# Kernel optimization log

Measured on AMD Instinct MI355X. Metric: run time of the kernel, lower is better.

Reference implementation:

```python
import jax, jax.numpy as jnp
import numpy as np

D_MODEL = 1024
N_HEADS = 16
D_K = D_MODEL // N_HEADS


def setup_inputs() -> dict:
    key = jax.random.key(0)
    ks = jax.random.split(key, 9)
    B, S = 4, 2048
    scale = 0.02
    x = jax.random.normal(ks[0], (B, S, D_MODEL), dtype=jnp.float32)
    mask = jnp.ones((1, 1, S, S), dtype=jnp.int32)
    wq = jax.random.normal(ks[1], (D_MODEL, D_MODEL), dtype=jnp.float32) * scale
    bq = jnp.zeros((D_MODEL,), dtype=jnp.float32)
    wk = jax.random.normal(ks[2], (D_MODEL, D_MODEL), dtype=jnp.float32) * scale
    bk = jnp.zeros((D_MODEL,), dtype=jnp.float32)
    wv = jax.random.normal(ks[3], (D_MODEL, D_MODEL), dtype=jnp.float32) * scale
    bv = jnp.zeros((D_MODEL,), dtype=jnp.float32)
    wo = jax.random.normal(ks[4], (D_MODEL, D_MODEL), dtype=jnp.float32) * scale
    bo = jnp.zeros((D_MODEL,), dtype=jnp.float32)
    return {"x": x, "mask": mask, "wq": wq, "bq": bq, "wk": wk, "bk": bk,
            "wv": wv, "bv": bv, "wo": wo, "bo": bo}


def reference(x, mask, wq, bq, wk, bk, wv, bv, wo, bo):
    B, S, _ = x.shape
    # torch Linear: y = x @ W.T + b
    def proj(w, b):
        return (jnp.einsum('bsd,ed->bse', x, w) + b).reshape(B, S, N_HEADS, D_K).transpose(0, 2, 1, 3)
    q = proj(wq, bq)  # [B,H,S,Dk]
    k = proj(wk, bk)
    v = proj(wv, bv)
    scores = jnp.einsum('bhqd,bhkd->bhqk', q, k) / jnp.sqrt(jnp.float32(D_K))
    scores = jnp.where(mask == 0, jnp.float32(-jnp.inf), scores)
    attn = jax.nn.softmax(scores, axis=-1)
    out = jnp.einsum('bhqk,bhkd->bhqd', attn, v)  # [B,H,S,Dk]
    out = out.transpose(0, 2, 1, 3).reshape(B, S, D_MODEL)
    return jnp.einsum('bsd,ed->bse', out, wo) + bo
```

## Files before the change

kernel.cpp:

```cpp
#include <hip/hip_runtime.h>
#include <hip/hip_bf16.h>
#include <math.h>
#include <stdint.h>

typedef unsigned short u16;
typedef unsigned int u32;
typedef __bf16 bf16x2 __attribute__((ext_vector_type(2)));
typedef __bf16 bf16x8 __attribute__((ext_vector_type(8)));
typedef float f32x4 __attribute__((ext_vector_type(4)));

#define AS1 __attribute__((address_space(1)))
#define AS3 __attribute__((address_space(3)))

#define QSCALE 0.18033688011112042f

__device__ __forceinline__ u16 f2bf(float f) {
  union { float f; u32 i; } c; c.f = f;
  const u32 x = c.i;
  return (u16)((x + 0x7fffu + ((x >> 16) & 1u)) >> 16);
}
#if __has_builtin(__builtin_amdgcn_cvt_pk_bf16_f32)
__device__ __forceinline__ u32 pkbf(float a, float b) {
  const bf16x2 v = __builtin_amdgcn_cvt_pk_bf16_f32(a, b);
  union { bf16x2 v; u32 i; } c; c.v = v; return c.i;
}
#else
__device__ __forceinline__ u32 pkbf(float a, float b) {
  return (u32)f2bf(a) | ((u32)f2bf(b) << 16);
}
#endif
#if __has_builtin(__builtin_amdgcn_exp2f)
#define EXP2(x) __builtin_amdgcn_exp2f(x)
#else
#define EXP2(x) __expf((x) * 0.6931471805599453f)
#endif
__device__ __forceinline__ void gload_lds16(const void* g, void* lds) {
  __builtin_amdgcn_global_load_lds((const AS1 void*)g, (AS3 void*)lds, 16, 0, 0);
}

__global__ void cast_all_kernel(const float* __restrict__ x, const float* __restrict__ wq,
                                const float* __restrict__ wk, const float* __restrict__ wv,
                                const float* __restrict__ wo, u16* __restrict__ xh,
                                u16* __restrict__ wh) {
  const int i = blockIdx.x * 256 + threadIdx.x;
  const float* src; u16* dst; int off;
  if (i < 2097152) {
    src = x; dst = xh; off = i;
  } else {
    const int j = i - 2097152;
    const int w = j >> 18;
    off = j & 262143;
    src = (w == 0) ? wq : (w == 1) ? wk : (w == 2) ? wv : wo;
    dst = wh + (size_t)w * 1048576;
  }
  const float4 v = ((const float4*)src)[off];
  ushort4 o;
  o.x = f2bf(v.x); o.y = f2bf(v.y); o.z = f2bf(v.z); o.w = f2bf(v.w);
  ((ushort4*)dst)[off] = o;
}

template <int MODE, bool SCALE>
__device__ __forceinline__ void gemm_body(const u16* __restrict__ A,
                                          const u16* __restrict__ W,
                                          const float* __restrict__ bias,
                                          void* __restrict__ out) {
  __shared__ alignas(16) u16 As[128 * 32];
  __shared__ alignas(16) u16 Bs[128 * 32];
  const int tid = threadIdx.x;
  const int wave = tid >> 6, lane = tid & 63;
  const int quad = lane >> 4, l16 = lane & 15;
  const int m0 = blockIdx.y * 128, n0 = blockIdx.x * 128;
  const int wm = (wave >> 1) * 64, wn = (wave & 1) * 64;

  f32x4 vzero = {0.f, 0.f, 0.f, 0.f};
  f32x4 acc[4][4];
#pragma unroll
  for (int i = 0; i < 4; i++)
#pragma unroll
    for (int j = 0; j < 4; j++) acc[i][j] = vzero;

  for (int k0 = 0; k0 < 1024; k0 += 32) {
#pragma unroll
    for (int p = 0; p < 2; ++p) {
      const int cbase = p * 256 + wave * 64;
      const int c = cbase + lane;
      const int row = c >> 2, kc4 = c & 3;
      gload_lds16(A + (size_t)(m0 + row) * 1024 + k0 + kc4 * 8, (char*)As + cbase * 16);
      gload_lds16(W + (size_t)(n0 + row) * 1024 + k0 + kc4 * 8, (char*)Bs + cbase * 16);
    }
    __syncthreads();
    bf16x8 af[4], bw[4];
#pragma unroll
    for (int im = 0; im < 4; im++)
      af[im] = *(const bf16x8*)&As[(wm + im * 16 + l16) * 32 + quad * 8];
#pragma unroll
    for (int in_ = 0; in_ < 4; in_++)
      bw[in_] = *(const bf16x8*)&Bs[(wn + in_ * 16 + l16) * 32 + quad * 8];
#pragma unroll
    for (int im = 0; im < 4; im++)
#pragma unroll
      for (int in_ = 0; in_ < 4; in_++)
        acc[im][in_] = __builtin_amdgcn_mfma_f32_16x16x32_bf16(af[im], bw[in_], acc[im][in_], 0, 0, 0);
    __syncthreads();
  }

#pragma unroll
  for (int in_ = 0; in_ < 4; in_++) {
    const int col = n0 + wn + in_ * 16 + l16;
    const float bvf = bias[col];
    if (MODE == 2) {
      const int h = col >> 6, dk = col & 63;
#pragma unroll
      for (int im = 0; im < 4; im++) {
        const int row0 = m0 + wm + im * 16 + quad * 4;
        const int b = row0 >> 11, s = row0 & 2047;
        const u32 lo = pkbf(acc[im][in_][0] + bvf, acc[im][in_][1] + bvf);
        const u32 hi = pkbf(acc[im][in_][2] + bvf, acc[im][in_][3] + bvf);
        u16* base = (u16*)out + ((size_t)(b * 16 + h) * 64 + dk) * 2048 + s;
        uint2 pkd; pkd.x = lo; pkd.y = hi;
        *(uint2*)base = pkd;
      }
    } else {
#pragma unroll
      for (int im = 0; im < 4; im++) {
#pragma unroll
        for (int r = 0; r < 4; r++) {
          const int row = m0 + wm + im * 16 + quad * 4 + r;
          float v = acc[im][in_][r] + bvf;
          if (SCALE) v *= QSCALE;
          if (MODE == 0) {
            ((float*)out)[(size_t)row * 1024 + col] = v;
          } else {
            const int b = row >> 11, s = row & 2047;
            const int h = col >> 6, dk = col & 63;
            ((u16*)out)[((((size_t)b * 16 + h) * 2048) + s) * 64 + dk] = f2bf(v);
          }
        }
      }
    }
  }
}

__global__ __launch_bounds__(256) void gemm_qkv_kernel(
    const u16* __restrict__ x, const u16* __restrict__ wq, const u16* __restrict__ wk,
    const u16* __restrict__ wv, const float* __restrict__ bq, const float* __restrict__ bk,
    const float* __restrict__ bv, u16* __restrict__ Q, u16* __restrict__ K,
    u16* __restrict__ VT) {
  if (blockIdx.z == 0)      gemm_body<1, true >(x, wq, bq, Q);
  else if (blockIdx.z == 1) gemm_body<1, false>(x, wk, bk, K);
  else                      gemm_body<2, false>(x, wv, bv, VT);
}

__global__ __launch_bounds__(256) void gemm_o_kernel(const u16* __restrict__ A,
                                                     const u16* __restrict__ wo,
                                                     const float* __restrict__ bo,
                                                     float* __restrict__ out) {
  gemm_body<0, false>(A, wo, bo, out);
}

__global__ void mask_check_kernel(const int* __restrict__ mask, int* __restrict__ flag) {
  const int i = blockIdx.x * 256 + threadIdx.x;
  const int4 v = ((const int4*)mask)[i];
  if (v.x == 0 || v.y == 0 || v.z == 0 || v.w == 0) atomicOr(flag, 1);
}

__global__ __launch_bounds__(256) void attn_kernel(const u16* __restrict__ Q,
                                                   const u16* __restrict__ K,
                                                   const u16* __restrict__ VT,
                                                   const int* __restrict__ mask,
                                                   const int* __restrict__ flag,
                                                   u16* __restrict__ O) {
  __shared__ alignas(16) u16 Ks[64 * 64];
  __shared__ alignas(16) u16 Vt[64 * 64];
  __shared__ alignas(16) u16 Ps[4 * 2048];

  const int tid = threadIdx.x;
  const int wave = tid >> 6, lane = tid & 63;
  const int quad = lane >> 4, l16 = lane & 15;
  const int qt_ = blockIdx.x, bh = blockIdx.y;
  const int b = bh >> 4, h = bh & 15;
  const int q0 = qt_ * 128;
  const u16* Qh = Q + (size_t)bh * 2048 * 64;
  const u16* Kh = K + (size_t)bh * 2048 * 64;
  const u16* Vth = VT + (size_t)bh * 64 * 2048;
  u16* Pw = Ps + wave * 2048;
  const bool masked = (*flag != 0);

  bf16x8 aq[2][2];
#pragma unroll
  for (int qt = 0; qt < 2; qt++) {
    const u16* qrow = Qh + (size_t)(q0 + qt * 64 + wave * 16 + l16) * 64 + quad * 8;
    aq[qt][0] = *(const bf16x8*)qrow;
    aq[qt][1] = *(const bf16x8*)(qrow + 32);
  }

  f32x4 vzero = {0.f, 0.f, 0.f, 0.f};
  f32x4 acc[2][4];
#pragma unroll
  for (int qt = 0; qt < 2; qt++)
#pragma unroll
    for (int jd = 0; jd < 4; jd++) acc[qt][jd] = vzero;
  float lp[2][4] = {{0.f, 0.f, 0.f, 0.f}, {0.f, 0.f, 0.f, 0.f}};

  for (int kb = 0; kb < 32; ++kb) {
    const int key0 = kb * 64;
#pragma unroll
    for (int p = 0; p < 2; ++p) {
      const int cbase = p * 256 + wave * 64;
      const int c = cbase + lane;
      const int row = c >> 3, cc = c & 7;
      gload_lds16(Kh + (size_t)(key0 + row) * 64 + ((cc ^ (row & 7)) << 3),
                  (char*)Ks + cbase * 16);
      gload_lds16(Vth + (size_t)row * 2048 + key0 + ((cc ^ (row & 7)) << 3),
                  (char*)Vt + cbase * 16);
    }
    __syncthreads();

#pragma unroll
    for (int jn = 0; jn < 4; jn++) {
      f32x4 sc0 = vzero, sc1 = vzero;
#pragma unroll
      for (int kc = 0; kc < 2; kc++) {
        const int r_ = jn * 16 + l16;
        const bf16x8 bk_ = *(const bf16x8*)
            &Ks[r_ * 64 + (((kc * 4 + quad) ^ (l16 & 7)) << 3)];
        sc0 = __builtin_amdgcn_mfma_f32_16x16x32_bf16(aq[0][kc], bk_, sc0, 0, 0, 0);
        sc1 = __builtin_amdgcn_mfma_f32_16x16x32_bf16(aq[1][kc], bk_, sc1, 0, 0, 0);
      }
      if (masked) {
#pragma unroll
        for (int r = 0; r < 4; r++) {
          const int kg = key0 + jn * 16 + l16;
          const int qa = q0 + wave * 16 + quad * 4 + r;
          if (mask[(size_t)qa * 2048 + kg] == 0) sc0[r] = -INFINITY;
          if (mask[(size_t)(qa + 64) * 2048 + kg] == 0) sc1[r] = -INFINITY;
        }
      }
      float pe0[4], pe1[4];
#pragma unroll
      for (int r = 0; r < 4; r++) {
        pe0[r] = EXP2(sc0[r]); lp[0][r] += pe0[r];
        pe1[r] = EXP2(sc1[r]); lp[1][r] += pe1[r];
      }
#pragma unroll
      for (int r = 0; r < 4; r += 2) {
        const u32 pk0 = pkbf(pe0[r], pe0[r + 1]);
        const u32 pk1 = pkbf(pe1[r], pe1[r + 1]);
        const int qa = quad * 4 + r, qb = qa + 1;
        const int sw = jn * 2 + (l16 >> 3), lo3 = l16 & 7;
        Pw[qa * 64 + (((sw ^ (qa & 7)) << 3)) + lo3] = (u16)pk0;
        Pw[qb * 64 + (((sw ^ (qb & 7)) << 3)) + lo3] = (u16)(pk0 >> 16);
        Pw[(16 + qa) * 64 + (((sw ^ (qa & 7)) << 3)) + lo3] = (u16)pk1;
        Pw[(16 + qb) * 64 + (((sw ^ (qb & 7)) << 3)) + lo3] = (u16)(pk1 >> 16);
      }
    }

    bf16x8 ap0[2], ap1[2];
#pragma unroll
    for (int kc = 0; kc < 2; kc++) {
      ap0[kc] = *(const bf16x8*)&Pw[l16 * 64 + (((kc * 4 + quad) ^ (l16 & 7)) << 3)];
      ap1[kc] = *(const bf16x8*)&Pw[(16 + l16) * 64 + (((kc * 4 + quad) ^ (l16 & 7)) << 3)];
    }
#pragma unroll
    for (int jd = 0; jd < 4; jd++) {
#pragma unroll
      for (int kc = 0; kc < 2; kc++) {
        const int dk_ = jd * 16 + l16;
        const bf16x8 bv_ = *(const bf16x8*)
            &Vt[dk_ * 64 + (((kc * 4 + quad) ^ (l16 & 7)) << 3)];
        acc[0][jd] = __builtin_amdgcn_mfma_f32_16x16x32_bf16(ap0[kc], bv_, acc[0][jd], 0, 0, 0);
        acc[1][jd] = __builtin_amdgcn_mfma_f32_16x16x32_bf16(ap1[kc], bv_, acc[1][jd], 0, 0, 0);
      }
    }
    __syncthreads();
  }

#pragma unroll
  for (int qt = 0; qt < 2; qt++) {
#pragma unroll
    for (int r = 0; r < 4; r++) {
      float ls = lp[qt][r];
#pragma unroll
      for (int off = 1; off < 16; off <<= 1) ls += __shfl_xor(ls, off, 16);
      const float linv = 1.0f / ls;
      const int qg = q0 + qt * 64 + wave * 16 + quad * 4 + r;
      const size_t token = (size_t)b * 2048 + qg;
#pragma unroll
      for (int jd = 0; jd < 4; jd++) {
        const int col = h * 64 + jd * 16 + l16;
        O[token * 1024 + col] = f2bf(acc[qt][jd][r] * linv);
      }
    }
  }
}

extern "C" void kernel_launch(void* const* d_in, const int* in_sizes, int n_in,
                              void* d_out, int out_size, void* d_ws, size_t ws_size,
                              hipStream_t stream) {
  const float* x  = (const float*)d_in[0];
  const int* mask = (const int*)d_in[1];
  const float* wq = (const float*)d_in[2];
  const float* bq = (const float*)d_in[3];
  const float* wk = (const float*)d_in[4];
  const float* bk = (const float*)d_in[5];
  const float* wv = (const float*)d_in[6];
  const float* bv = (const float*)d_in[7];
  const float* wo = (const float*)d_in[8];
  const float* bo = (const float*)d_in[9];
  float* out = (float*)d_out;

  u16* xh = (u16*)d_ws;
  u16* wh = xh + 8388608;
  u16* Qw = wh + 4194304;
  u16* Kw = Qw + 8388608;
  u16* Vw = Kw + 8388608;
  int* mflag = (int*)(Vw + 8388608);
  u16* Ow = xh;

  hipMemsetAsync(mflag, 0, sizeof(int), stream);
  mask_check_kernel<<<4096, 256, 0, stream>>>(mask, mflag);
  cast_all_kernel<<<12288, 256, 0, stream>>>(x, wq, wk, wv, wo, xh, wh);

  gemm_qkv_kernel<<<dim3(8, 64, 3), 256, 0, stream>>>(
      xh, wh + 0 * 1048576, wh + 1 * 1048576, wh + 2 * 1048576,
      bq, bk, bv, Qw, Kw, Vw);
  attn_kernel<<<dim3(16, 64), 256, 0, stream>>>(Qw, Kw, Vw, mask, mflag, Ow);
  gemm_o_kernel<<<dim3(8, 64, 1), 256, 0, stream>>>(Ow, wh + 3 * 1048576, bo, out);
}
```

Baseline: 339.9 us.

## Double-buffer K/V tiles in attention kernel to overlap loads with compute

Moves the K and V^T shared-memory tiles into two-slot global LDS arrays. The key-block loop is unrolled by two so the async global-to-LDS load of the next tile is issued before computing on the current one. The aim is to hide global load latency behind the MFMA and softmax work instead of stalling at each barrier. In exchange, LDS use per block rises from 32KB to 48KB, which may reduce occupancy.

```diff
diff --git a/kernel.cpp b/kernel.cpp
--- a/kernel.cpp
+++ b/kernel.cpp
@@ -164,32 +164,122 @@
   if (v.x == 0 || v.y == 0 || v.z == 0 || v.w == 0) atomicOr(flag, 1);
 }
 
+struct AttnState {
+  const u16* Kh; const u16* Vth;
+  int wave, lane, quad, l16, q0;
+  bool masked; const int* mask; int bh;
+};
+
+__shared__ alignas(16) u16 Ks_s[2][4096];
+__shared__ alignas(16) u16 Vt_s[2][4096];
+__shared__ alignas(16) u16 Ps_s[4][2048];
+
+__device__ __forceinline__ void attn_stage(const AttnState& st, int kb, int buf) {
+  const int key0 = kb * 64;
+#pragma unroll
+  for (int p = 0; p < 2; ++p) {
+    const int cbase = p * 256 + st.wave * 64;
+    const int c = cbase + st.lane;
+    const int row = c >> 3, cc = c & 7;
+    gload_lds16(st.Kh + (size_t)(key0 + row) * 64 + ((cc ^ (row & 7)) << 3),
+                (char*)&Ks_s[buf][0] + cbase * 16);
+    gload_lds16(st.Vth + (size_t)row * 2048 + key0 + ((cc ^ (row & 7)) << 3),
+                (char*)&Vt_s[buf][0] + cbase * 16);
+  }
+}
+
+__device__ __forceinline__ void attn_iter(const AttnState& st, int kb, int cur,
+                                          const bf16x8 aq[2][2], f32x4 acc[2][4],
+                                          float lp[2][4]) {
+  const int wave = st.wave, quad = st.quad, l16 = st.l16;
+  u16* Pw = &Ps_s[wave][0];
+  const u16* Ksc = &Ks_s[cur][0];
+  const u16* Vtc = &Vt_s[cur][0];
+  const int key0 = kb * 64;
+  f32x4 vzero = {0.f, 0.f, 0.f, 0.f};
+
+#pragma unroll
+  for (int jn = 0; jn < 4; jn++) {
+    f32x4 sc0 = vzero, sc1 = vzero;
+#pragma unroll
+    for (int kc = 0; kc < 2; kc++) {
+      const int r_ = jn * 16 + l16;
+      const bf16x8 bk_ = *(const bf16x8*)
+          &Ksc[r_ * 64 + (((kc * 4 + quad) ^ (l16 & 7)) << 3)];
+      sc0 = __builtin_amdgcn_mfma_f32_16x16x32_bf16(aq[0][kc], bk_, sc0, 0, 0, 0);
+      sc1 = __builtin_amdgcn_mfma_f32_16x16x32_bf16(aq[1][kc], bk_, sc1, 0, 0, 0);
+    }
+    if (st.masked) {
+#pragma unroll
+      for (int r = 0; r < 4; r++) {
+        const int kg = key0 + jn * 16 + l16;
+        const int qa = st.q0 + wave * 16 + quad * 4 + r;
+        if (st.mask[(size_t)qa * 2048 + kg] == 0) sc0[r] = -INFINITY;
+        if (st.mask[(size_t)(qa + 64) * 2048 + kg] == 0) sc1[r] = -INFINITY;
+      }
+    }
+    float pe0[4], pe1[4];
+#pragma unroll
+    for (int r = 0; r < 4; r++) {
+      pe0[r] = EXP2(sc0[r]); lp[0][r] += pe0[r];
+      pe1[r] = EXP2(sc1[r]); lp[1][r] += pe1[r];
+    }
+#pragma unroll
+    for (int r = 0; r < 4; r += 2) {
+      const u32 pk0 = pkbf(pe0[r], pe0[r + 1]);
+      const u32 pk1 = pkbf(pe1[r], pe1[r + 1]);
+      const int qa = quad * 4 + r, qb = qa + 1;
+      const int sw = jn * 2 + (l16 >> 3), lo3 = l16 & 7;
+      Pw[qa * 64 + (((sw ^ (qa & 7)) << 3)) + lo3] = (u16)pk0;
+      Pw[qb * 64 + (((sw ^ (qb & 7)) << 3)) + lo3] = (u16)(pk0 >> 16);
+      Pw[(16 + qa) * 64 + (((sw ^ (qa & 7)) << 3)) + lo3] = (u16)pk1;
+      Pw[(16 + qb) * 64 + (((sw ^ (qb & 7)) << 3)) + lo3] = (u16)(pk1 >> 16);
+    }
+  }
+
+  bf16x8 ap0[2], ap1[2];
+#pragma unroll
+  for (int kc = 0; kc < 2; kc++) {
+    ap0[kc] = *(const bf16x8*)&Pw[l16 * 64 + (((kc * 4 + quad) ^ (l16 & 7)) << 3)];
+    ap1[kc] = *(const bf16x8*)&Pw[(16 + l16) * 64 + (((kc * 4 + quad) ^ (l16 & 7)) << 3)];
+  }
+#pragma unroll
+  for (int jd = 0; jd < 4; jd++) {
+#pragma unroll
+    for (int kc = 0; kc < 2; kc++) {
+      const int dk_ = jd * 16 + l16;
+      const bf16x8 bv_ = *(const bf16x8*)
+          &Vtc[dk_ * 64 + (((kc * 4 + quad) ^ (l16 & 7)) << 3)];
+      acc[0][jd] = __builtin_amdgcn_mfma_f32_16x16x32_bf16(ap0[kc], bv_, acc[0][jd], 0, 0, 0);
+      acc[1][jd] = __builtin_amdgcn_mfma_f32_16x16x32_bf16(ap1[kc], bv_, acc[1][jd], 0, 0, 0);
+    }
+  }
+}
+
 __global__ __launch_bounds__(256) void attn_kernel(const u16* __restrict__ Q,
                                                    const u16* __restrict__ K,
                                                    const u16* __restrict__ VT,
                                                    const int* __restrict__ mask,
                                                    const int* __restrict__ flag,
                                                    u16* __restrict__ O) {
-  __shared__ alignas(16) u16 Ks[64 * 64];
-  __shared__ alignas(16) u16 Vt[64 * 64];
-  __shared__ alignas(16) u16 Ps[4 * 2048];
-
   const int tid = threadIdx.x;
-  const int wave = tid >> 6, lane = tid & 63;
-  const int quad = lane >> 4, l16 = lane & 15;
-  const int qt_ = blockIdx.x, bh = blockIdx.y;
-  const int b = bh >> 4, h = bh & 15;
-  const int q0 = qt_ * 128;
-  const u16* Qh = Q + (size_t)bh * 2048 * 64;
-  const u16* Kh = K + (size_t)bh * 2048 * 64;
-  const u16* Vth = VT + (size_t)bh * 64 * 2048;
-  u16* Pw = Ps + wave * 2048;
-  const bool masked = (*flag != 0);
+  AttnState st;
+  st.wave = tid >> 6; st.lane = tid & 63;
+  st.quad = st.lane >> 4; st.l16 = st.lane & 15;
+  const int qt_ = blockIdx.x;
+  st.bh = blockIdx.y;
+  const int b = st.bh >> 4, h = st.bh & 15;
+  st.q0 = qt_ * 128;
+  const u16* Qh = Q + (size_t)st.bh * 2048 * 64;
+  st.Kh = K + (size_t)st.bh * 2048 * 64;
+  st.Vth = VT + (size_t)st.bh * 64 * 2048;
+  st.mask = mask;
+  st.masked = (*flag != 0);
 
   bf16x8 aq[2][2];
 #pragma unroll
   for (int qt = 0; qt < 2; qt++) {
-    const u16* qrow = Qh + (size_t)(q0 + qt * 64 + wave * 16 + l16) * 64 + quad * 8;
+    const u16* qrow = Qh + (size_t)(st.q0 + qt * 64 + st.wave * 16 + st.l16) * 64 + st.quad * 8;
     aq[qt][0] = *(const bf16x8*)qrow;
     aq[qt][1] = *(const bf16x8*)(qrow + 32);
   }
@@ -202,77 +292,15 @@
     for (int jd = 0; jd < 4; jd++) acc[qt][jd] = vzero;
   float lp[2][4] = {{0.f, 0.f, 0.f, 0.f}, {0.f, 0.f, 0.f, 0.f}};
 
-  for (int kb = 0; kb < 32; ++kb) {
-    const int key0 = kb * 64;
-#pragma unroll
-    for (int p = 0; p < 2; ++p) {
-      const int cbase = p * 256 + wave * 64;
-      const int c = cbase + lane;
-      const int row = c >> 3, cc = c & 7;
-      gload_lds16(Kh + (size_t)(key0 + row) * 64 + ((cc ^ (row & 7)) << 3),
-                  (char*)Ks + cbase * 16);
-      gload_lds16(Vth + (size_t)row * 2048 + key0 + ((cc ^ (row & 7)) << 3),
-                  (char*)Vt + cbase * 16);
-    }
+  attn_stage(st, 0, 0);
+  for (int kbp = 0; kbp < 16; kbp++) {
+    const int kb0 = kbp * 2;
     __syncthreads();
-
-#pragma unroll
-    for (int jn = 0; jn < 4; jn++) {
-      f32x4 sc0 = vzero, sc1 = vzero;
-#pragma unroll
-      for (int kc = 0; kc < 2; kc++) {
-        const int r_ = jn * 16 + l16;
-        const bf16x8 bk_ = *(const bf16x8*)
-            &Ks[r_ * 64 + (((kc * 4 + quad) ^ (l16 & 7)) << 3)];
-        sc0 = __builtin_amdgcn_mfma_f32_16x16x32_bf16(aq[0][kc], bk_, sc0, 0, 0, 0);
-        sc1 = __builtin_amdgcn_mfma_f32_16x16x32_bf16(aq[1][kc], bk_, sc1, 0, 0, 0);
-      }
-      if (masked) {
-#pragma unroll
-        for (int r = 0; r < 4; r++) {
-          const int kg = key0 + jn * 16 + l16;
-          const int qa = q0 + wave * 16 + quad * 4 + r;
-          if (mask[(size_t)qa * 2048 + kg] == 0) sc0[r] = -INFINITY;
-          if (mask[(size_t)(qa + 64) * 2048 + kg] == 0) sc1[r] = -INFINITY;
-        }
-      }
-      float pe0[4], pe1[4];
-#pragma unroll
-      for (int r = 0; r < 4; r++) {
-        pe0[r] = EXP2(sc0[r]); lp[0][r] += pe0[r];
-        pe1[r] = EXP2(sc1[r]); lp[1][r] += pe1[r];
-      }
-#pragma unroll
-      for (int r = 0; r < 4; r += 2) {
-        const u32 pk0 = pkbf(pe0[r], pe0[r + 1]);
-        const u32 pk1 = pkbf(pe1[r], pe1[r + 1]);
-        const int qa = quad * 4 + r, qb = qa + 1;
-        const int sw = jn * 2 + (l16 >> 3), lo3 = l16 & 7;
-        Pw[qa * 64 + (((sw ^ (qa & 7)) << 3)) + lo3] = (u16)pk0;
-        Pw[qb * 64 + (((sw ^ (qb & 7)) << 3)) + lo3] = (u16)(pk0 >> 16);
-        Pw[(16 + qa) * 64 + (((sw ^ (qa & 7)) << 3)) + lo3] = (u16)pk1;
-        Pw[(16 + qb) * 64 + (((sw ^ (qb & 7)) << 3)) + lo3] = (u16)(pk1 >> 16);
-      }
-    }
-
-    bf16x8 ap0[2], ap1[2];
-#pragma unroll
-    for (int kc = 0; kc < 2; kc++) {
-      ap0[kc] = *(const bf16x8*)&Pw[l16 * 64 + (((kc * 4 + quad) ^ (l16 & 7)) << 3)];
-      ap1[kc] = *(const bf16x8*)&Pw[(16 + l16) * 64 + (((kc * 4 + quad) ^ (l16 & 7)) << 3)];
-    }
-#pragma unroll
-    for (int jd = 0; jd < 4; jd++) {
-#pragma unroll
-      for (int kc = 0; kc < 2; kc++) {
-        const int dk_ = jd * 16 + l16;
-        const bf16x8 bv_ = *(const bf16x8*)
-            &Vt[dk_ * 64 + (((kc * 4 + quad) ^ (l16 & 7)) << 3)];
-        acc[0][jd] = __builtin_amdgcn_mfma_f32_16x16x32_bf16(ap0[kc], bv_, acc[0][jd], 0, 0, 0);
-        acc[1][jd] = __builtin_amdgcn_mfma_f32_16x16x32_bf16(ap1[kc], bv_, acc[1][jd], 0, 0, 0);
-      }
-    }
+    attn_stage(st, kb0 + 1, 1);
+    attn_iter(st, kb0, 0, aq, acc, lp);
     __syncthreads();
+    if (kbp < 15) attn_stage(st, kb0 + 2, 0);
+    attn_iter(st, kb0 + 1, 1, aq, acc, lp);
   }
 
 #pragma unroll
@@ -283,11 +311,11 @@
 #pragma unroll
       for (int off = 1; off < 16; off <<= 1) ls += __shfl_xor(ls, off, 16);
       const float linv = 1.0f / ls;
-      const int qg = q0 + qt * 64 + wave * 16 + quad * 4 + r;
+      const int qg = st.q0 + qt * 64 + st.wave * 16 + st.quad * 4 + r;
       const size_t token = (size_t)b * 2048 + qg;
 #pragma unroll
       for (int jd = 0; jd < 4; jd++) {
-        const int col = h * 64 + jd * 16 + l16;
+        const int col = h * 64 + jd * 16 + st.l16;
         O[token * 1024 + col] = f2bf(acc[qt][jd][r] * linv);
       }
     }
```

After: 345.7 us. About the same (+1.7%).
